# Kernel optimization log

Hardware: AMD Instinct MI355X
Metric: run time of the kernel (lower is better)

Reference implementation:

```python
import jax, jax.numpy as jnp
import numpy as np

N, E, D_IN, D_H, N_CLS, N_GRAPHS = 50000, 1600000, 128, 64, 10, 64
NEG_SLOPE = 0.2


def _glorot(key, shape):
    fan_in = shape[0]
    return (jax.random.normal(key, shape, dtype=jnp.float32) * np.sqrt(1.0 / fan_in)).astype(jnp.float32)


def setup_inputs() -> dict:
    key = jax.random.key(0)
    ks = jax.random.split(key, 20)
    inp = {
        "x": jax.random.normal(ks[0], (N, D_IN), dtype=jnp.float32),
        "edge_index": jax.random.randint(ks[1], (2, E), 0, N, dtype=jnp.int64) if jax.config.jax_enable_x64 else jax.random.randint(ks[1], (2, E), 0, N).astype(jnp.int32),
        "edge_attr": jax.random.uniform(ks[2], (E, 1), dtype=jnp.float32),
        "batch": jnp.sort(jax.random.randint(ks[3], (N,), 0, N_GRAPHS)),
        # conv1 params
        "Wl1": _glorot(ks[4], (D_IN, D_H)), "bl1": jnp.zeros((D_H,), jnp.float32),
        "Wr1": _glorot(ks[5], (D_IN, D_H)), "br1": jnp.zeros((D_H,), jnp.float32),
        "We1": _glorot(ks[6], (1, D_H)),
        "att1": _glorot(ks[7], (D_H,)),
        "b1": jnp.zeros((D_H,), jnp.float32),
        # conv2 params
        "Wl2": _glorot(ks[8], (D_H, D_H)), "bl2": jnp.zeros((D_H,), jnp.float32),
        "Wr2": _glorot(ks[9], (D_H, D_H)), "br2": jnp.zeros((D_H,), jnp.float32),
        "We2": _glorot(ks[10], (1, D_H)),
        "att2": _glorot(ks[11], (D_H,)),
        "b2": jnp.zeros((D_H,), jnp.float32),
        # classifier
        "Wc": _glorot(ks[12], (D_H, N_CLS)), "bc": jnp.zeros((N_CLS,), jnp.float32),
    }
    return inp


def _segment_softmax(logits, seg, num_segments):
    m = jax.ops.segment_max(logits, seg, num_segments=num_segments)
    z = jnp.exp(logits - m[seg])
    s = jax.ops.segment_sum(z, seg, num_segments=num_segments)
    return z / (s[seg] + 1e-16)


def _gatv2(x, src, dst, eattr, Wl, bl, Wr, br, We, att, b):
    # PyG GATv2Conv, heads=1, add_self_loops=True (fill_value='mean'), eval mode
    xl = x @ Wl + bl  # source-side transform [N, D]
    xr = x @ Wr + br  # target-side transform [N, D]
    loop = jnp.arange(N, dtype=src.dtype)
    src2 = jnp.concatenate([src, loop])
    dst2 = jnp.concatenate([dst, loop])
    loop_attr = jnp.broadcast_to(eattr.mean(axis=0, keepdims=True), (N, eattr.shape[1]))
    ea2 = jnp.concatenate([eattr, loop_attr], axis=0) @ We  # [E+N, D]
    msg = jax.nn.leaky_relu(xl[src2] + xr[dst2] + ea2, NEG_SLOPE)  # [E+N, D]
    logits = msg @ att  # [E+N]
    alpha = _segment_softmax(logits, dst2, N)
    out = jax.ops.segment_sum(xl[src2] * alpha[:, None], dst2, num_segments=N)
    return out + b


def reference(x, edge_index, edge_attr, batch,
              Wl1, bl1, Wr1, br1, We1, att1, b1,
              Wl2, bl2, Wr2, br2, We2, att2, b2,
              Wc, bc):
    src, dst = edge_index[0], edge_index[1]
    h = jax.nn.elu(_gatv2(x, src, dst, edge_attr, Wl1, bl1, Wr1, br1, We1, att1, b1))
    # dropout p=0.2 is identity in eval mode
    h = jax.nn.elu(_gatv2(h, src, dst, edge_attr, Wl2, bl2, Wr2, br2, We2, att2, b2))
    # global mean pool per graph
    sums = jax.ops.segment_sum(h, batch, num_segments=N_GRAPHS)
    counts = jax.ops.segment_sum(jnp.ones((N,), h.dtype), batch, num_segments=N_GRAPHS)
    pooled = sums / jnp.maximum(counts, 1.0)[:, None]  # [G, D_H]
    return pooled @ Wc + bc
```

## Files before the change

### kernel.cpp

```cpp
#include <hip/hip_runtime.h>
#include <hip/hip_fp16.h>
#include <math.h>

#define N_NODES 50000
#define N_EDGES 1600000
#define D_IN 128
#define D_H 64
#define N_CLS 10
#define N_GRAPHS 64
#define NEG_SLOPE 0.2f
#define E2 (N_EDGES + N_NODES)
#define SCAN_BS 256
#define NBLK ((N_NODES + SCAN_BS - 1) / SCAN_BS)

#define NB 25
#define BSH 11
#define CAP 76800
#define HBB 8
#define EPT 8
#define PAD 32
#define SLICES 8
#define SLICE_W (2048 / SLICES)

typedef _Float16 f16x2 __attribute__((ext_vector_type(2)));

__device__ inline f16x2 as_h2(unsigned u) { return __builtin_bit_cast(f16x2, u); }
__device__ inline int h2_as_int(f16x2 v) { return __builtin_bit_cast(int, v); }

__device__ inline f16x2 pk_leaky(f16x2 m, f16x2 ns) {
#if __has_builtin(__builtin_elementwise_max)
    return __builtin_elementwise_max(m, m * ns);
#else
    f16x2 p = m * ns, r;
    r.x = m.x > p.x ? m.x : p.x;
    r.y = m.y > p.y ? m.y : p.y;
    return r;
#endif
}

#if __has_builtin(__builtin_amdgcn_fdot2)
__device__ inline float fdot2a(f16x2 a, f16x2 b, float c) {
    return __builtin_amdgcn_fdot2(a, b, c, false);
}
#else
__device__ inline float fdot2a(f16x2 a, f16x2 b, float c) {
    return fmaf((float)a.x, (float)b.x, fmaf((float)a.y, (float)b.y, c));
}
#endif

__device__ inline float wave_reduce_sum(float v) {
    for (int off = 32; off; off >>= 1) v += __shfl_xor(v, off);
    return v;
}

__global__ void bucket_stage(const int* __restrict__ src, const int* __restrict__ dst,
                             const float* __restrict__ eattr,
                             float* esum, int* bcursor,
                             int2* __restrict__ stg) {
    __shared__ int bcnt[4][32];
    __shared__ int woff[4][32];
    __shared__ float esh[4];
    int t = threadIdx.x;
    int wave = t >> 6;
    if (t < 128) bcnt[t >> 5][t & 31] = 0;
    __syncthreads();
    int e0 = (blockIdx.x * blockDim.x + t) * EPT;
    int ss[EPT], tt[EPT], aa[EPT], r[EPT], b[EPT];
    float v = 0.f;
    bool valid = e0 < N_EDGES;
    if (valid) {
        #pragma unroll
        for (int q = 0; q < EPT / 4; ++q) {
            int4 s4 = *(const int4*)(src + e0 + 4 * q);
            int4 t4 = *(const int4*)(dst + e0 + 4 * q);
            float4 a4 = *(const float4*)(eattr + e0 + 4 * q);
            ss[4*q] = s4.x; ss[4*q+1] = s4.y; ss[4*q+2] = s4.z; ss[4*q+3] = s4.w;
            tt[4*q] = t4.x; tt[4*q+1] = t4.y; tt[4*q+2] = t4.z; tt[4*q+3] = t4.w;
            aa[4*q]   = h2_as_int((f16x2){(_Float16)a4.x, (_Float16)a4.x});
            aa[4*q+1] = h2_as_int((f16x2){(_Float16)a4.y, (_Float16)a4.y});
            aa[4*q+2] = h2_as_int((f16x2){(_Float16)a4.z, (_Float16)a4.z});
            aa[4*q+3] = h2_as_int((f16x2){(_Float16)a4.w, (_Float16)a4.w});
            v += (a4.x + a4.y) + (a4.z + a4.w);
        }
        #pragma unroll
        for (int i = 0; i < EPT; ++i) {
            b[i] = tt[i] >> BSH;
            r[i] = atomicAdd(&bcnt[wave][b[i]], 1);
        }
    }
    v = wave_reduce_sum(v);
    if ((t & 63) == 0) esh[wave] = v;
    __syncthreads();
    if (t < NB) {
        int c0 = bcnt[0][t], c1 = bcnt[1][t], c2 = bcnt[2][t], c3 = bcnt[3][t];
        int tot = c0 + c1 + c2 + c3;
        int base = tot ? atomicAdd(&bcursor[t * PAD], tot) : 0;
        woff[0][t] = base;
        woff[1][t] = base + c0;
        woff[2][t] = base + c0 + c1;
        woff[3][t] = base + c0 + c1 + c2;
    }
    if (t == 0) {
        float tot = (esh[0] + esh[1]) + (esh[2] + esh[3]);
        atomicAdd(&esum[(blockIdx.x & 31) * PAD], tot);
    }
    __syncthreads();
    if (valid) {
        #pragma unroll
        for (int i = 0; i < EPT; ++i) {
            int p = b[i] * CAP + woff[wave][b[i]] + r[i];
            stg[p] = make_int2((ss[i] & 0xFFFF) | ((tt[i] & 2047) << 16), aa[i]);
        }
    }
}

__global__ void hist_bucket(const int2* __restrict__ stg, const int* __restrict__ bcursor,
                            int* cnt) {
    __shared__ int hist[2048];
    int b = blockIdx.x / HBB;
    int j = blockIdx.x % HBB;
    for (int i = threadIdx.x; i < 2048; i += 256) hist[i] = 0;
    __syncthreads();
    int n = bcursor[b * PAD];
    const int2* sd = stg + (size_t)b * CAP;
    int per = (n + HBB - 1) / HBB;
    int start = j * per;
    int end = min(start + per, n);
    for (int idx = start + threadIdx.x; idx < end; idx += 256)
        atomicAdd(&hist[(sd[idx].x >> 16) & 2047], 1);
    __syncthreads();
    int nb = b << BSH;
    for (int i = threadIdx.x; i < 2048; i += 256) {
        int c = hist[i];
        if (c) atomicAdd(&cnt[nb + i], c);
    }
}

__global__ void scan_block(const int* __restrict__ cnt, int* __restrict__ row_start,
                           int* __restrict__ partial) {
    __shared__ int sd[SCAN_BS];
    int i = blockIdx.x * SCAN_BS + threadIdx.x;
    int v = (i < N_NODES) ? (cnt[i] + 1) : 0;
    sd[threadIdx.x] = v;
    __syncthreads();
    for (int off = 1; off < SCAN_BS; off <<= 1) {
        int t = (threadIdx.x >= off) ? sd[threadIdx.x - off] : 0;
        __syncthreads();
        sd[threadIdx.x] += t;
        __syncthreads();
    }
    if (i < N_NODES) row_start[i] = sd[threadIdx.x] - v;
    if (threadIdx.x == SCAN_BS - 1) partial[blockIdx.x] = sd[threadIdx.x];
}
__global__ void add_offsets(int* __restrict__ row_start, const int* __restrict__ partial,
                            int* __restrict__ cursor, const float* __restrict__ esum,
                            int2* __restrict__ csr_pack) {
    __shared__ int sp[SCAN_BS];
    int pv = (threadIdx.x < NBLK) ? partial[threadIdx.x] : 0;
    sp[threadIdx.x] = pv;
    __syncthreads();
    for (int off = 1; off < SCAN_BS; off <<= 1) {
        int t = (threadIdx.x >= off) ? sp[threadIdx.x - off] : 0;
        __syncthreads();
        sp[threadIdx.x] += t;
        __syncthreads();
    }
    float es = 0.f;
    #pragma unroll
    for (int jj = 0; jj < 32; ++jj) es += esum[jj * PAD];
    float esm = es * (1.0f / N_EDGES);
    int ebits = h2_as_int((f16x2){(_Float16)esm, (_Float16)esm});
    int base = (blockIdx.x == 0) ? 0 : sp[blockIdx.x - 1];
    int i = blockIdx.x * SCAN_BS + threadIdx.x;
    if (i < N_NODES) {
        int r = row_start[i] + base;
        row_start[i] = r;
        csr_pack[r] = make_int2(i, ebits);
        cursor[i] = r + 1;
    }
    if (i == 0) row_start[N_NODES] = E2;
}

__global__ __launch_bounds__(1024) void scatter_slice(
                              const int2* __restrict__ stg,
                              const int* __restrict__ bcursor,
                              const int* __restrict__ row_start,
                              int2* __restrict__ csr_pack) {
    __shared__ int lcur[SLICE_W];
    int b = blockIdx.x & 31;
    int m = blockIdx.x >> 5;
    if (b >= NB) return;
    int nbase = (b << BSH) + m * SLICE_W;
    for (int i = threadIdx.x; i < SLICE_W; i += 1024) {
        int node = nbase + i;
        lcur[i] = (node < N_NODES) ? row_start[node] + 1 : 0;
    }
    __syncthreads();
    int n = bcursor[b * PAD];
    const int4* sd4 = (const int4*)(stg + (size_t)b * CAP);
    int n4 = n >> 1;
    int lo = m * SLICE_W, hi = lo + SLICE_W;
    for (int base4 = 0; base4 < n4; base4 += 4096) {
        int4 e[4];
        int idx[4];
        #pragma unroll
        for (int j = 0; j < 4; ++j) {
            idx[j] = base4 + j * 1024 + (int)threadIdx.x;
            if (idx[j] < n4) e[j] = sd4[idx[j]];
        }
        #pragma unroll
        for (int j = 0; j < 4; ++j) {
            if (idx[j] < n4) {
                int dl0 = (e[j].x >> 16) & 2047;
                if (dl0 >= lo && dl0 < hi) {
                    int q = atomicAdd(&lcur[dl0 - lo], 1);
                    csr_pack[q] = make_int2(e[j].x & 0xFFFF, e[j].y);
                }
                int dl1 = (e[j].z >> 16) & 2047;
                if (dl1 >= lo && dl1 < hi) {
                    int q = atomicAdd(&lcur[dl1 - lo], 1);
                    csr_pack[q] = make_int2(e[j].z & 0xFFFF, e[j].w);
                }
            }
        }
    }
    if ((n & 1) && threadIdx.x == 0) {
        int2 e = stg[(size_t)b * CAP + n - 1];
        int dl = (e.x >> 16) & 2047;
        if (dl >= lo && dl < hi) {
            int q = atomicAdd(&lcur[dl - lo], 1);
            csr_pack[q] = make_int2(e.x & 0xFFFF, e.y);
        }
    }
}

template<int K>
__global__ __launch_bounds__(256) void linear_dual_k(
                              const float* __restrict__ x,
                              const float* __restrict__ Wl, const float* __restrict__ bl,
                              const float* __restrict__ Wr, const float* __restrict__ br,
                              __half* __restrict__ xl, __half* __restrict__ xr) {
    const int TN = 64;
    const int NPW = TN / 4;
    __shared__ float xs[TN * K];
    int t = threadIdx.x;
    int nb = blockIdx.x * TN;
    int rem = N_NODES - nb;
    int tot4 = (rem >= TN ? TN : rem) * (K / 4);
    const float4* xg = (const float4*)(x + (size_t)nb * K);
    float4* xs4 = (float4*)xs;
    for (int i = t; i < tot4; i += 256) xs4[i] = xg[i];
    __syncthreads();
    int wave = t >> 6, d = t & 63;
    int n0 = wave * NPW;
    float blv = bl[d], brv = br[d];
    float al[NPW], ar[NPW];
    #pragma unroll
    for (int i = 0; i < NPW; ++i) { al[i] = blv; ar[i] = brv; }
    #pragma unroll 2
    for (int k4 = 0; k4 < K / 4; ++k4) {
        int kb = k4 * 4;
        float wl[4], wr[4];
        #pragma unroll
        for (int q = 0; q < 4; ++q) {
            wl[q] = Wl[(kb + q) * D_H + d];
            wr[q] = Wr[(kb + q) * D_H + d];
        }
        #pragma unroll
        for (int i = 0; i < NPW; ++i) {
            float4 xv = *(const float4*)&xs[(n0 + i) * K + kb];
            al[i] = fmaf(xv.x, wl[0], al[i]);
            al[i] = fmaf(xv.y, wl[1], al[i]);
            al[i] = fmaf(xv.z, wl[2], al[i]);
            al[i] = fmaf(xv.w, wl[3], al[i]);
            ar[i] = fmaf(xv.x, wr[0], ar[i]);
            ar[i] = fmaf(xv.y, wr[1], ar[i]);
            ar[i] = fmaf(xv.z, wr[2], ar[i]);
            ar[i] = fmaf(xv.w, wr[3], ar[i]);
        }
    }
    #pragma unroll
    for (int i = 0; i < NPW; ++i) {
        int g = nb + n0 + i;
        if (g < N_NODES) {
            xl[(size_t)g * D_H + d] = __float2half(al[i]);
            xr[(size_t)g * D_H + d] = __float2half(ar[i]);
        }
    }
}

__global__ __launch_bounds__(256) void gat_fused(
        const int* __restrict__ row_start, const int2* __restrict__ csr_pack,
        const __half* __restrict__ xl, const __half* __restrict__ xr,
        const float* __restrict__ We, const float* __restrict__ att,
        const float* __restrict__ b, float* __restrict__ out) {
    int lane = threadIdx.x & 63;
    int g = lane >> 4;
    int s = lane & 15;
    int wid = blockIdx.x * (blockDim.x >> 6) + (threadIdx.x >> 6);
    int node = wid * 4 + g;
    bool nv = node < N_NODES;
    int nodec = nv ? node : 0;
    int fb = s * 4;
    float4 we4  = *(const float4*)(We + fb);
    float4 att4 = *(const float4*)(att + fb);
    f16x2 we0 = {(_Float16)we4.x, (_Float16)we4.y};
    f16x2 we1 = {(_Float16)we4.z, (_Float16)we4.w};
    f16x2 at0 = {(_Float16)att4.x, (_Float16)att4.y};
    f16x2 at1 = {(_Float16)att4.z, (_Float16)att4.w};
    uint2 xru = *(const uint2*)(xr + (size_t)nodec * D_H + fb);
    f16x2 xr0 = as_h2(xru.x), xr1 = as_h2(xru.y);
    const f16x2 ns = {(_Float16)NEG_SLOPE, (_Float16)NEG_SLOPE};
    int j0 = 0, j1 = 0;
    if (nv) { j0 = row_start[node]; j1 = row_start[node + 1]; }

    float S = 0.f;
    float4 acc = make_float4(0.f, 0.f, 0.f, 0.f);

    for (int i0 = j0; i0 < j1; i0 += 4) {
        int2 pk[4]; uint2 qk[4]; bool vk[4];
        #pragma unroll
        for (int k = 0; k < 4; ++k) {
            vk[k] = (i0 + k) < j1;
            int c = vk[k] ? (i0 + k) : i0;
            pk[k] = csr_pack[c];
        }
        #pragma unroll
        for (int k = 0; k < 4; ++k)
            qk[k] = *(const uint2*)(xl + (size_t)pk[k].x * D_H + fb);
        float t[4]; f16x2 rl[4], rh[4];
        #pragma unroll
        for (int k = 0; k < 4; ++k) {
            rl[k] = as_h2(qk[k].x);
            rh[k] = as_h2(qk[k].y);
            f16x2 a2 = as_h2((unsigned)pk[k].y);
            f16x2 m0 = a2 * we0 + (rl[k] + xr0);
            f16x2 m1 = a2 * we1 + (rh[k] + xr1);
            m0 = pk_leaky(m0, ns);
            m1 = pk_leaky(m1, ns);
            t[k] = fdot2a(m1, at1, fdot2a(m0, at0, 0.f));
        }
        #pragma unroll
        for (int off = 1; off <= 8; off <<= 1) {
            t[0] += __shfl_xor(t[0], off);
            t[1] += __shfl_xor(t[1], off);
            t[2] += __shfl_xor(t[2], off);
            t[3] += __shfl_xor(t[3], off);
        }
        float z[4];
        #pragma unroll
        for (int k = 0; k < 4; ++k)
            z[k] = vk[k] ? __expf(t[k]) : 0.f;
        S += (z[0] + z[1]) + (z[2] + z[3]);
        #pragma unroll
        for (int k = 0; k < 4; ++k) {
            acc.x = fmaf(z[k], (float)rl[k].x, acc.x);
            acc.y = fmaf(z[k], (float)rl[k].y, acc.y);
            acc.z = fmaf(z[k], (float)rh[k].x, acc.z);
            acc.w = fmaf(z[k], (float)rh[k].y, acc.w);
        }
    }

    if (nv) {
        float4 b4 = *(const float4*)(b + fb);
        float inv = 1.f / (S + 1e-16f);
        float4 h;
        h.x = fmaf(acc.x, inv, b4.x);
        h.y = fmaf(acc.y, inv, b4.y);
        h.z = fmaf(acc.z, inv, b4.z);
        h.w = fmaf(acc.w, inv, b4.w);
        h.x = h.x > 0.f ? h.x : expm1f(h.x);
        h.y = h.y > 0.f ? h.y : expm1f(h.y);
        h.z = h.z > 0.f ? h.z : expm1f(h.z);
        h.w = h.w > 0.f ? h.w : expm1f(h.w);
        *(float4*)(out + (size_t)node * D_H + fb) = h;
    }
}

__global__ void pool(const float* __restrict__ h, const int* __restrict__ batch,
                     float* __restrict__ pooled, float* __restrict__ counts) {
    const int CHUNK = 128;
    int base = blockIdx.x * CHUNK;
    int d = threadIdx.x;
    float accv = 0.f; int cur_g = -1; int cnt = 0;
    for (int i = 0; i < CHUNK; ++i) {
        int n = base + i;
        if (n >= N_NODES) break;
        int g = batch[n];
        if (g != cur_g) {
            if (cur_g >= 0) {
                atomicAdd(&pooled[cur_g * D_H + d], accv);
                if (d == 0) atomicAdd(&counts[cur_g], (float)cnt);
            }
            cur_g = g; accv = 0.f; cnt = 0;
        }
        accv += h[(size_t)n * D_H + d];
        cnt++;
    }
    if (cur_g >= 0) {
        atomicAdd(&pooled[cur_g * D_H + d], accv);
        if (d == 0) atomicAdd(&counts[cur_g], (float)cnt);
    }
}

__global__ void classify(const float* __restrict__ pooled, const float* __restrict__ counts,
                         const float* __restrict__ Wc, const float* __restrict__ bc,
                         float* __restrict__ out) {
    int tid = threadIdx.x;
    int g = tid / N_CLS, c = tid % N_CLS;
    if (g >= N_GRAPHS) return;
    float inv = 1.0f / fmaxf(counts[g], 1.0f);
    float a = bc[c];
    for (int k = 0; k < D_H; ++k)
        a = fmaf(pooled[g * D_H + k] * inv, Wc[k * N_CLS + c], a);
    out[g * N_CLS + c] = a;
}

extern "C" void kernel_launch(void* const* d_in, const int* in_sizes, int n_in,
                              void* d_out, int out_size, void* d_ws, size_t ws_size,
                              hipStream_t stream) {
    const float* x     = (const float*)d_in[0];
    const int*   ei    = (const int*)d_in[1];
    const float* eattr = (const float*)d_in[2];
    const int*   batch = (const int*)d_in[3];
    const float *Wl1 = (const float*)d_in[4],  *bl1 = (const float*)d_in[5];
    const float *Wr1 = (const float*)d_in[6],  *br1 = (const float*)d_in[7];
    const float *We1 = (const float*)d_in[8],  *att1 = (const float*)d_in[9];
    const float *b1  = (const float*)d_in[10];
    const float *Wl2 = (const float*)d_in[11], *bl2 = (const float*)d_in[12];
    const float *Wr2 = (const float*)d_in[13], *br2 = (const float*)d_in[14];
    const float *We2 = (const float*)d_in[15], *att2 = (const float*)d_in[16];
    const float *b2  = (const float*)d_in[17];
    const float *Wc  = (const float*)d_in[18], *bc = (const float*)d_in[19];
    float* out = (float*)d_out;

    const int* src = ei;
    const int* dst = ei + N_EDGES;

    char* base = (char*)d_ws;
    int2*  stg     = (int2*)base;
    __half* xl     = (__half*)base;
    __half* xr     = xl + (size_t)N_NODES * D_H;
    float* h       = (float*)(xr + (size_t)N_NODES * D_H);
    int2*  csr_pack = (int2*)(base + (size_t)NB * CAP * 16);
    int*   row_start = (int*)(csr_pack + E2);
    int*   cnt     = row_start + N_NODES + 1;
    float* esum    = (float*)(cnt + N_NODES);
    int*   bcursor = (int*)(esum + 32 * PAD);
    int*   cursor  = bcursor + NB * PAD;
    int*   partial = cursor + N_NODES;
    float* pooled  = (float*)(partial + NBLK);
    float* counts  = pooled + N_GRAPHS * D_H;

    int gat_blocks = (N_NODES + 15) / 16;
    int lin_blocks = (N_NODES + 63) / 64;

    hipMemsetAsync(cnt, 0, (N_NODES + 32 * PAD + NB * PAD) * sizeof(int), stream);
    hipMemsetAsync(pooled, 0, (N_GRAPHS * D_H + N_GRAPHS) * sizeof(float), stream);

    bucket_stage<<<(N_EDGES / EPT + 255) / 256, 256, 0, stream>>>(
        src, dst, eattr, esum, bcursor, stg);
    hist_bucket<<<NB * HBB, 256, 0, stream>>>(stg, bcursor, cnt);
    scan_block<<<NBLK, SCAN_BS, 0, stream>>>(cnt, row_start, partial);
    add_offsets<<<NBLK, SCAN_BS, 0, stream>>>(row_start, partial, cursor, esum, csr_pack);
    scatter_slice<<<SLICES * 32, 1024, 0, stream>>>(stg, bcursor, row_start, csr_pack);

    linear_dual_k<D_IN><<<lin_blocks, 256, 0, stream>>>(x, Wl1, bl1, Wr1, br1, xl, xr);
    gat_fused<<<gat_blocks, 256, 0, stream>>>(row_start, csr_pack, xl, xr, We1, att1, b1, h);

    linear_dual_k<D_H><<<lin_blocks, 256, 0, stream>>>(h, Wl2, bl2, Wr2, br2, xl, xr);
    gat_fused<<<gat_blocks, 256, 0, stream>>>(row_start, csr_pack, xl, xr, We2, att2, b2, h);

    pool<<<(N_NODES + 127) / 128, 64, 0, stream>>>(h, batch, pooled, counts);
    classify<<<1, 640, 0, stream>>>(pooled, counts, Wc, bc, out);
}
```

Before: 367.4 us.

## Restructure dual linear, widen GAT edge batch to 8, shrink pool chunks

```diff
diff --git a/kernel.cpp b/kernel.cpp
--- a/kernel.cpp
+++ b/kernel.cpp
@@ -240,52 +240,56 @@
                               const float* __restrict__ Wl, const float* __restrict__ bl,
                               const float* __restrict__ Wr, const float* __restrict__ br,
                               __half* __restrict__ xl, __half* __restrict__ xr) {
-    const int TN = 64;
-    const int NPW = TN / 4;
-    __shared__ float xs[TN * K];
-    int t = threadIdx.x;
-    int nb = blockIdx.x * TN;
-    int rem = N_NODES - nb;
-    int tot4 = (rem >= TN ? TN : rem) * (K / 4);
-    const float4* xg = (const float4*)(x + (size_t)nb * K);
-    float4* xs4 = (float4*)xs;
-    for (int i = t; i < tot4; i += 256) xs4[i] = xg[i];
-    __syncthreads();
-    int wave = t >> 6, d = t & 63;
-    int n0 = wave * NPW;
-    float blv = bl[d], brv = br[d];
-    float al[NPW], ar[NPW];
+    int lane = threadIdx.x & 63;
+    int wave = threadIdx.x >> 6;
+    int dg = (lane & 7) * 8;
+    int node = blockIdx.x * 32 + wave * 8 + (lane >> 3);
+    bool nv = node < N_NODES;
+    const float* xrow = x + (size_t)(nv ? node : 0) * K;
+    float al[8], ar[8];
     #pragma unroll
-    for (int i = 0; i < NPW; ++i) { al[i] = blv; ar[i] = brv; }
-    #pragma unroll 2
+    for (int j = 0; j < 8; ++j) { al[j] = bl[dg + j]; ar[j] = br[dg + j]; }
     for (int k4 = 0; k4 < K / 4; ++k4) {
         int kb = k4 * 4;
-        float wl[4], wr[4];
+        float4 xv = *(const float4*)(xrow + kb);
+        float xq[4] = {xv.x, xv.y, xv.z, xv.w};
         #pragma unroll
         for (int q = 0; q < 4; ++q) {
-            wl[q] = Wl[(kb + q) * D_H + d];
-            wr[q] = Wr[(kb + q) * D_H + d];
-        }
-        #pragma unroll
-        for (int i = 0; i < NPW; ++i) {
-            float4 xv = *(const float4*)&xs[(n0 + i) * K + kb];
-            al[i] = fmaf(xv.x, wl[0], al[i]);
-            al[i] = fmaf(xv.y, wl[1], al[i]);
-            al[i] = fmaf(xv.z, wl[2], al[i]);
-            al[i] = fmaf(xv.w, wl[3], al[i]);
-            ar[i] = fmaf(xv.x, wr[0], ar[i]);
-            ar[i] = fmaf(xv.y, wr[1], ar[i]);
-            ar[i] = fmaf(xv.z, wr[2], ar[i]);
-            ar[i] = fmaf(xv.w, wr[3], ar[i]);
-        }
-    }
-    #pragma unroll
-    for (int i = 0; i < NPW; ++i) {
-        int g = nb + n0 + i;
-        if (g < N_NODES) {
-            xl[(size_t)g * D_H + d] = __float2half(al[i]);
-            xr[(size_t)g * D_H + d] = __float2half(ar[i]);
-        }
+            float4 wla = *(const float4*)(Wl + (kb + q) * D_H + dg);
+            float4 wlb = *(const float4*)(Wl + (kb + q) * D_H + dg + 4);
+            float4 wra = *(const float4*)(Wr + (kb + q) * D_H + dg);
+            float4 wrb = *(const float4*)(Wr + (kb + q) * D_H + dg + 4);
+            al[0] = fmaf(xq[q], wla.x, al[0]);
+            al[1] = fmaf(xq[q], wla.y, al[1]);
+            al[2] = fmaf(xq[q], wla.z, al[2]);
+            al[3] = fmaf(xq[q], wla.w, al[3]);
+            al[4] = fmaf(xq[q], wlb.x, al[4]);
+            al[5] = fmaf(xq[q], wlb.y, al[5]);
+            al[6] = fmaf(xq[q], wlb.z, al[6]);
+            al[7] = fmaf(xq[q], wlb.w, al[7]);
+            ar[0] = fmaf(xq[q], wra.x, ar[0]);
+            ar[1] = fmaf(xq[q], wra.y, ar[1]);
+            ar[2] = fmaf(xq[q], wra.z, ar[2]);
+            ar[3] = fmaf(xq[q], wra.w, ar[3]);
+            ar[4] = fmaf(xq[q], wrb.x, ar[4]);
+            ar[5] = fmaf(xq[q], wrb.y, ar[5]);
+            ar[6] = fmaf(xq[q], wrb.z, ar[6]);
+            ar[7] = fmaf(xq[q], wrb.w, ar[7]);
+        }
+    }
+    if (nv) {
+        int4 pl = make_int4(
+            h2_as_int((f16x2){(_Float16)al[0], (_Float16)al[1]}),
+            h2_as_int((f16x2){(_Float16)al[2], (_Float16)al[3]}),
+            h2_as_int((f16x2){(_Float16)al[4], (_Float16)al[5]}),
+            h2_as_int((f16x2){(_Float16)al[6], (_Float16)al[7]}));
+        int4 pr = make_int4(
+            h2_as_int((f16x2){(_Float16)ar[0], (_Float16)ar[1]}),
+            h2_as_int((f16x2){(_Float16)ar[2], (_Float16)ar[3]}),
+            h2_as_int((f16x2){(_Float16)ar[4], (_Float16)ar[5]}),
+            h2_as_int((f16x2){(_Float16)ar[6], (_Float16)ar[7]}));
+        *(int4*)(xl + (size_t)node * D_H + dg) = pl;
+        *(int4*)(xr + (size_t)node * D_H + dg) = pr;
     }
 }
 
@@ -317,20 +321,20 @@
     float S = 0.f;
     float4 acc = make_float4(0.f, 0.f, 0.f, 0.f);
 
-    for (int i0 = j0; i0 < j1; i0 += 4) {
-        int2 pk[4]; uint2 qk[4]; bool vk[4];
-        #pragma unroll
-        for (int k = 0; k < 4; ++k) {
+    for (int i0 = j0; i0 < j1; i0 += 8) {
+        int2 pk[8]; uint2 qk[8]; bool vk[8];
+        #pragma unroll
+        for (int k = 0; k < 8; ++k) {
             vk[k] = (i0 + k) < j1;
             int c = vk[k] ? (i0 + k) : i0;
             pk[k] = csr_pack[c];
         }
         #pragma unroll
-        for (int k = 0; k < 4; ++k)
+        for (int k = 0; k < 8; ++k)
             qk[k] = *(const uint2*)(xl + (size_t)pk[k].x * D_H + fb);
-        float t[4]; f16x2 rl[4], rh[4];
-        #pragma unroll
-        for (int k = 0; k < 4; ++k) {
+        float t[8]; f16x2 rl[8], rh[8];
+        #pragma unroll
+        for (int k = 0; k < 8; ++k) {
             rl[k] = as_h2(qk[k].x);
             rh[k] = as_h2(qk[k].y);
             f16x2 a2 = as_h2((unsigned)pk[k].y);
@@ -342,18 +346,16 @@
         }
         #pragma unroll
         for (int off = 1; off <= 8; off <<= 1) {
-            t[0] += __shfl_xor(t[0], off);
-            t[1] += __shfl_xor(t[1], off);
-            t[2] += __shfl_xor(t[2], off);
-            t[3] += __shfl_xor(t[3], off);
-        }
-        float z[4];
-        #pragma unroll
-        for (int k = 0; k < 4; ++k)
+            #pragma unroll
+            for (int k = 0; k < 8; ++k) t[k] += __shfl_xor(t[k], off);
+        }
+        float z[8];
+        #pragma unroll
+        for (int k = 0; k < 8; ++k)
             z[k] = vk[k] ? __expf(t[k]) : 0.f;
-        S += (z[0] + z[1]) + (z[2] + z[3]);
-        #pragma unroll
-        for (int k = 0; k < 4; ++k) {
+        #pragma unroll
+        for (int k = 0; k < 8; ++k) {
+            S += z[k];
             acc.x = fmaf(z[k], (float)rl[k].x, acc.x);
             acc.y = fmaf(z[k], (float)rl[k].y, acc.y);
             acc.z = fmaf(z[k], (float)rh[k].x, acc.z);
@@ -379,7 +381,7 @@
 
 __global__ void pool(const float* __restrict__ h, const int* __restrict__ batch,
                      float* __restrict__ pooled, float* __restrict__ counts) {
-    const int CHUNK = 128;
+    const int CHUNK = 32;
     int base = blockIdx.x * CHUNK;
     int d = threadIdx.x;
     float accv = 0.f; int cur_g = -1; int cnt = 0;
@@ -453,7 +455,7 @@
     float* counts  = pooled + N_GRAPHS * D_H;
 
     int gat_blocks = (N_NODES + 15) / 16;
-    int lin_blocks = (N_NODES + 63) / 64;
+    int lin_blocks = (N_NODES + 31) / 32;
 
     hipMemsetAsync(cnt, 0, (N_NODES + 32 * PAD + NB * PAD) * sizeof(int), stream);
     hipMemsetAsync(pooled, 0, (N_GRAPHS * D_H + N_GRAPHS) * sizeof(float), stream);
@@ -471,6 +473,6 @@
     linear_dual_k<D_H><<<lin_blocks, 256, 0, stream>>>(h, Wl2, bl2, Wr2, br2, xl, xr);
     gat_fused<<<gat_blocks, 256, 0, stream>>>(row_start, csr_pack, xl, xr, We2, att2, b2, h);
 
-    pool<<<(N_NODES + 127) / 128, 64, 0, stream>>>(h, batch, pooled, counts);
+    pool<<<(N_NODES + 31) / 32, 64, 0, stream>>>(h, batch, pooled, counts);
     classify<<<1, 640, 0, stream>>>(pooled, counts, Wc, bc, out);
 }
```

New measurement: 449.2 us. 22.3% more time.
